# Performance work log

Measured on AMD Instinct MI355X. Metric: run time of the kernel, lower is better.

Reference implementation:

```python
import jax, jax.numpy as jnp
import numpy as np

N = 200000   # lane-graph nodes
C = 128      # n_map
S = 6        # num_scales
EP = 100000  # edges per pre/suc scale
EL = 25000   # left/right edges
EPS = 1e-5


def gn1(x, g, b):
    # GroupNorm(1, C) over shape [N, C]: normalize per node across channels, affine per channel
    mu = jnp.mean(x, axis=-1, keepdims=True)
    var = jnp.mean(jnp.square(x - mu), axis=-1, keepdims=True)
    return (x - mu) * jax.lax.rsqrt(var + EPS) * g + b


def setup_inputs() -> dict:
    key = jax.random.key(0)
    ks = jax.random.split(key, 32)
    f = lambda i, shape, s=1.0: jax.random.normal(ks[i], shape, dtype=jnp.float32) * s
    sc = 1.0 / np.sqrt(C)
    inp = {
        'control':   f(0, (N,)),
        'turn':      f(1, (N, 2)),
        'intersect': f(2, (N,)),
        'ctrs':      f(3, (N, 2)),
        'feats':     f(4, (N, 2)),
        'pre':   jax.random.randint(ks[5], (S, 2, EP), 0, N, dtype=jnp.int32),
        'suc':   jax.random.randint(ks[6], (S, 2, EP), 0, N, dtype=jnp.int32),
        'left':  jax.random.randint(ks[7], (2, EL), 0, N, dtype=jnp.int32),
        'right': jax.random.randint(ks[8], (2, EL), 0, N, dtype=jnp.int32),
        # input branch: Linear(2,C)+b, ReLU, Linear(C,C,no bias)+GroupNorm(1,C)
        'w_in1': f(9, (2, C), 0.7), 'b_in1': jnp.zeros((C,), jnp.float32),
        'w_in2': f(10, (C, C), sc), 'gn_in_g': jnp.ones((C,), jnp.float32), 'gn_in_b': jnp.zeros((C,), jnp.float32),
        # seg branch
        'w_seg1': f(11, (2, C), 0.7), 'b_seg1': jnp.zeros((C,), jnp.float32),
        'w_seg2': f(12, (C, C), sc), 'gn_seg_g': jnp.ones((C,), jnp.float32), 'gn_seg_b': jnp.zeros((C,), jnp.float32),
        # meta: Linear(C+4,C,no bias)+GN+ReLU
        'w_meta': f(13, (C + 4, C), sc), 'gn_meta_g': jnp.ones((C,), jnp.float32), 'gn_meta_b': jnp.zeros((C,), jnp.float32),
        # fuse dict, 4 layers
        'ctr_w':   f(14, (4, C, C), sc),
        'pre_w':   f(15, (4, S, C, C), sc),
        'suc_w':   f(16, (4, S, C, C), sc),
        'left_w':  f(17, (4, C, C), sc),
        'right_w': f(18, (4, C, C), sc),
        'norm_g': jnp.ones((4, C), jnp.float32), 'norm_b': jnp.zeros((4, C), jnp.float32),
        'ctr2_w': f(19, (4, C, C), sc),
        'ctr2_g': jnp.ones((4, C), jnp.float32), 'ctr2_b': jnp.zeros((4, C), jnp.float32),
    }
    return inp


def reference(control, turn, intersect, ctrs, feats, pre, suc, left, right,
              w_in1, b_in1, w_in2, gn_in_g, gn_in_b,
              w_seg1, b_seg1, w_seg2, gn_seg_g, gn_seg_b,
              w_meta, gn_meta_g, gn_meta_b,
              ctr_w, pre_w, suc_w, left_w, right_w,
              norm_g, norm_b, ctr2_w, ctr2_g, ctr2_b):
    # input / seg branches
    a = gn1(jax.nn.relu(ctrs @ w_in1 + b_in1) @ w_in2, gn_in_g, gn_in_b)
    b = gn1(jax.nn.relu(feats @ w_seg1 + b_seg1) @ w_seg2, gn_seg_g, gn_seg_b)
    feat = jax.nn.relu(a + b)
    # meta fuse
    meta = jnp.concatenate([feat, turn, control[:, None], intersect[:, None]], axis=1)
    feat = jax.nn.relu(gn1(meta @ w_meta, gn_meta_g, gn_meta_b))
    res = feat
    for i in range(4):
        temp = feat @ ctr_w[i]
        # multi-scale pre/suc: gather -> per-scale linear -> scatter-add
        pre_msg = jnp.einsum('sec,scd->sed', feat[pre[:, 1]], pre_w[i])   # [S,EP,C]
        temp = temp.at[pre[:, 0].reshape(-1)].add(pre_msg.reshape(-1, C))
        suc_msg = jnp.einsum('sec,scd->sed', feat[suc[:, 1]], suc_w[i])
        temp = temp.at[suc[:, 0].reshape(-1)].add(suc_msg.reshape(-1, C))
        temp = temp.at[left[0]].add(feat[left[1]] @ left_w[i])
        temp = temp.at[right[0]].add(feat[right[1]] @ right_w[i])
        feat = jax.nn.relu(gn1(temp, norm_g[i], norm_b[i]))
        feat = gn1(feat @ ctr2_w[i], ctr2_g[i], ctr2_b[i])
        feat = jax.nn.relu(feat + res)
        res = feat
    return (feat, ctrs)
```

## Files before the change

### kernel.cpp

```cpp
#include <hip/hip_runtime.h>

#define N_NODES 200000
#define CDIM 128
#define NSCALE 6
#define NEP 100000
#define NEL 25000
#define NCLS 14
#define NCHUNK 196
#define MROWS 64

typedef unsigned short u16;
typedef unsigned int u32;

using fragAB = __attribute__((ext_vector_type(8))) short;
using fragC  = __attribute__((ext_vector_type(4))) float;

enum { P_PLAIN = 0, P_TWO = 1, P_META = 2 };
enum { E_GN = 1, E_RELU = 2 };

__device__ __forceinline__ float4 ld4(const float* p) { return *(const float4*)p; }

__device__ __forceinline__ u16 f2bf(float f) {
  u32 u = __builtin_bit_cast(u32, f);
  u = (u + 0x7fff + ((u >> 16) & 1)) >> 16;
  return (u16)u;
}
__device__ __forceinline__ u32 pk2(float a, float b) {
  return (u32)f2bf(a) | ((u32)f2bf(b) << 16);
}
__device__ __forceinline__ float bflo(u32 u) { return __builtin_bit_cast(float, u << 16); }
__device__ __forceinline__ float bfhi(u32 u) { return __builtin_bit_cast(float, u & 0xffff0000u); }

__device__ __forceinline__ void acc16(float* s, uint4 a, uint4 b) {
  s[0] += bflo(a.x); s[1] += bfhi(a.x); s[2]  += bflo(a.y); s[3]  += bfhi(a.y);
  s[4] += bflo(a.z); s[5] += bfhi(a.z); s[6]  += bflo(a.w); s[7]  += bfhi(a.w);
  s[8] += bflo(b.x); s[9] += bfhi(b.x); s[10] += bflo(b.y); s[11] += bfhi(b.y);
  s[12] += bflo(b.z); s[13] += bfhi(b.z); s[14] += bflo(b.w); s[15] += bfhi(b.w);
}

__host__ __device__ constexpr int idx_base(int c) {
  return (c < 12) ? c * NEP : 12 * NEP + (c - 12) * NEL;
}

__device__ __forceinline__ int wslot(int li, int c) {
  if (c < 0)  return 2 + li;
  if (c < 6)  return 18 + li * 6 + c;
  if (c < 12) return 42 + li * 6 + (c - 6);
  return (c == 12) ? (10 + li) : (14 + li);
}

template<int PRO, int EPI>
__global__ __launch_bounds__(256)
void mm_k(int M, int Kp,
          const float* __restrict__ Af, const float* __restrict__ A2f,
          const float* __restrict__ e0, const float* __restrict__ e1, const float* __restrict__ e2,
          const u16* __restrict__ Wt,
          float* __restrict__ Y, u16* __restrict__ Yb,
          const float* __restrict__ gn_g, const float* __restrict__ gn_b)
{
  constexpr int LSTR = 56;
  __shared__ u16 As[128 * LSTR];
  __shared__ u16 Bs[128 * LSTR];

  const int tid = threadIdx.x;
  const int lane = tid & 63, wid = tid >> 6;
  const int wm = (wid >> 1) * 64, wn = (wid & 1) * 64;
  const int q = lane >> 4, l16 = lane & 15;
  const int row0 = blockIdx.x * 128;
  const int srow = tid >> 1, shalf = tid & 1;

  fragC acc[4][4];
  #pragma unroll
  for (int i = 0; i < 4; i++)
    #pragma unroll
    for (int j = 0; j < 4; j++)
      #pragma unroll
      for (int e = 0; e < 4; e++) acc[i][j][e] = 0.0f;

  const int sgrow = row0 + srow;
  const bool svalid = (sgrow < M);
  float x0 = 0.f, x1 = 0.f, mx = 0.f, my = 0.f, mc = 0.f, mi = 0.f;
  if constexpr (PRO == P_TWO) {
    if (svalid) { x0 = Af[(size_t)sgrow * 2]; x1 = Af[(size_t)sgrow * 2 + 1]; }
  }
  if constexpr (PRO == P_META) {
    if (svalid) { mx = e0[(size_t)sgrow * 2]; my = e0[(size_t)sgrow * 2 + 1]; mc = e1[sgrow]; mi = e2[sgrow]; }
  }

  const int nk = Kp >> 5;
  for (int kt = 0; kt < nk; ++kt) {
    const int k0 = kt * 32 + shalf * 16;
    {
      u16* adst = &As[srow * LSTR + shalf * 16];
      float v[16];
      #pragma unroll
      for (int j = 0; j < 16; j++) v[j] = 0.f;
      if constexpr (PRO == P_TWO) {
        #pragma unroll
        for (int j0 = 0; j0 < 16; j0 += 4) {
          float4 wa = ld4(e0 + k0 + j0);
          float4 wb = ld4(e0 + 128 + k0 + j0);
          float4 bb = ld4(e1 + k0 + j0);
          v[j0]     = fmaxf(0.f, fmaf(x0, wa.x, fmaf(x1, wb.x, bb.x)));
          v[j0 + 1] = fmaxf(0.f, fmaf(x0, wa.y, fmaf(x1, wb.y, bb.y)));
          v[j0 + 2] = fmaxf(0.f, fmaf(x0, wa.z, fmaf(x1, wb.z, bb.z)));
          v[j0 + 3] = fmaxf(0.f, fmaf(x0, wa.w, fmaf(x1, wb.w, bb.w)));
        }
      } else {
        if (svalid) {
          if (k0 < 128) {
            const float* sa = Af + (size_t)sgrow * 128 + k0;
            const float* sb = A2f + (size_t)sgrow * 128 + k0;
            #pragma unroll
            for (int j0 = 0; j0 < 16; j0 += 4) {
              float4 a = ld4(sa + j0), b = ld4(sb + j0);
              v[j0]     = fmaxf(0.f, a.x + b.x);
              v[j0 + 1] = fmaxf(0.f, a.y + b.y);
              v[j0 + 2] = fmaxf(0.f, a.z + b.z);
              v[j0 + 3] = fmaxf(0.f, a.w + b.w);
            }
          } else {
            #pragma unroll
            for (int j = 0; j < 16; j++) {
              const int kk = k0 + j - 128;
              v[j] = (kk == 0) ? mx : (kk == 1) ? my : (kk == 2) ? mc : (kk == 3) ? mi : 0.f;
            }
          }
        }
      }
      u32 p[8];
      #pragma unroll
      for (int j = 0; j < 8; j++) p[j] = pk2(v[2 * j], v[2 * j + 1]);
      *(uint4*)adst = make_uint4(p[0], p[1], p[2], p[3]);
      *(uint4*)(adst + 8) = make_uint4(p[4], p[5], p[6], p[7]);
    }
    {
      const u16* s = Wt + (size_t)srow * Kp + k0;
      uint4 b0 = *(const uint4*)s, b1 = *(const uint4*)(s + 8);
      u16* bdst = &Bs[srow * LSTR + shalf * 16];
      *(uint4*)bdst = b0; *(uint4*)(bdst + 8) = b1;
    }
    __syncthreads();
    fragAB af[4], bf[4];
    #pragma unroll
    for (int t = 0; t < 4; t++) af[t] = *(const fragAB*)&As[(wm + t * 16 + l16) * LSTR + q * 8];
    #pragma unroll
    for (int t = 0; t < 4; t++) bf[t] = *(const fragAB*)&Bs[(wn + t * 16 + l16) * LSTR + q * 8];
    #pragma unroll
    for (int mt = 0; mt < 4; mt++)
      #pragma unroll
      for (int nt = 0; nt < 4; nt++)
        acc[mt][nt] = __builtin_amdgcn_mfma_f32_16x16x32_bf16(af[mt], bf[nt], acc[mt][nt], 0, 0, 0);
    __syncthreads();
  }

  __shared__ float2 red[128][2];
  __shared__ float2 stats[128];
  #pragma unroll
  for (int mt = 0; mt < 4; mt++)
    #pragma unroll
    for (int r = 0; r < 4; r++) {
      float s1 = acc[mt][0][r] + acc[mt][1][r] + acc[mt][2][r] + acc[mt][3][r];
      float s2 = acc[mt][0][r] * acc[mt][0][r] + acc[mt][1][r] * acc[mt][1][r]
               + acc[mt][2][r] * acc[mt][2][r] + acc[mt][3][r] * acc[mt][3][r];
      #pragma unroll
      for (int off = 1; off < 16; off <<= 1) {
        s1 += __shfl_xor(s1, off, 64);
        s2 += __shfl_xor(s2, off, 64);
      }
      if (l16 == 0) red[wm + mt * 16 + q * 4 + r][wid & 1] = make_float2(s1, s2);
    }
  __syncthreads();
  if (tid < 128) {
    const float2 p0 = red[tid][0], p1 = red[tid][1];
    const float m = (p0.x + p1.x) * (1.0f / 128.0f);
    const float var = (p0.y + p1.y) * (1.0f / 128.0f) - m * m;
    stats[tid] = make_float2(m, rsqrtf(var + 1e-5f));
  }
  __syncthreads();
  float gl[4], bl[4];
  #pragma unroll
  for (int nt = 0; nt < 4; nt++) {
    gl[nt] = gn_g[wn + nt * 16 + l16];
    bl[nt] = gn_b[wn + nt * 16 + l16];
  }
  #pragma unroll
  for (int mt = 0; mt < 4; mt++)
    #pragma unroll
    for (int r = 0; r < 4; r++) {
      const int rl = wm + mt * 16 + q * 4 + r;
      const int grow = row0 + rl;
      if (grow >= M) continue;
      const float2 st = stats[rl];
      #pragma unroll
      for (int nt = 0; nt < 4; nt++) {
        const int col = wn + nt * 16 + l16;
        float v = (acc[mt][nt][r] - st.x) * st.y * gl[nt] + bl[nt];
        if constexpr ((EPI & E_RELU) != 0) v = fmaxf(v, 0.f);
        if (Y)  Y[(size_t)grow * 128 + col] = v;
        if (Yb) Yb[(size_t)grow * 128 + col] = f2bf(v);
      }
    }
}

__global__ __launch_bounds__(256, 4)
void layer_k(const u16* __restrict__ Fin, u16* __restrict__ Fout,
             float* __restrict__ outf,
             const int* __restrict__ ptrs, const int* __restrict__ idxs,
             const u16* __restrict__ Wt, int li,
             const float* __restrict__ g1, const float* __restrict__ b1,
             const float* __restrict__ g2, const float* __restrict__ b2)
{
  __shared__ u16 ldsA[MROWS * 128];
  __shared__ u16 Bsb[128 * 32];
  __shared__ u16 ends[NCLS][MROWS];
  __shared__ int cbase[NCLS];
  __shared__ int ccnt[NCLS];
  __shared__ int idxC[2][256];

  float2* red   = (float2*)Bsb;
  float2* stats = (float2*)(Bsb + 512);

  const int tid = threadIdx.x;
  const int lane = tid & 63, wid = tid >> 6;
  const int wm = (wid >> 1) * 32, wn = (wid & 1) * 64;
  const int q = lane >> 4, l16 = lane & 15;
  const int row0 = blockIdx.x * MROWS;
  const int row8 = tid >> 3;
  const int goff = (tid & 7) * 16;

  auto swzA = [&](int row, int colu) -> u16* {
    u32 b = (u32)(row * 256 + colu * 2) ^ ((u32)(row & 7) << 4);
    return (u16*)((char*)ldsA + b);
  };
  auto swzB = [&](int row, int colu) -> u16* {
    u32 b = (u32)(row * 64 + colu * 2) ^ ((((u32)((row >> 1) ^ (row >> 3))) & 3u) << 4);
    return (u16*)((char*)Bsb + b);
  };

  fragC acc[2][4];
  #pragma unroll
  for (int i = 0; i < 2; i++)
    #pragma unroll
    for (int j = 0; j < 4; j++)
      #pragma unroll
      for (int e = 0; e < 4; e++) acc[i][j][e] = 0.0f;

  if (tid < NCLS) {
    const int* pc = ptrs + (size_t)tid * (N_NODES + 1);
    const int b = row0 ? pc[row0 - 1] : 0;
    const int hiRow = (row0 + MROWS - 1 < N_NODES) ? (row0 + MROWS - 1) : (N_NODES - 1);
    cbase[tid] = b;
    ccnt[tid] = pc[hiRow] - b;
  }
  __syncthreads();

  #pragma unroll 1
  for (int t = tid; t < NCLS * MROWS; t += 256) {
    const int c = t / MROWS, r = t % MROWS;
    const int grow = row0 + r;
    const int* pc = ptrs + (size_t)c * (N_NODES + 1);
    const int gr = (grow < N_NODES) ? grow : (N_NODES - 1);
    ends[c][r] = (u16)(pc[gr] - cbase[c]);
  }
  {
    const int srow4 = tid >> 2, q4 = tid & 3;
    const int sgrow = row0 + srow4;
    uint4 a[4];
    #pragma unroll
    for (int j = 0; j < 4; j++) a[j] = make_uint4(0, 0, 0, 0);
    if (sgrow < N_NODES) {
      const u16* s = Fin + (size_t)sgrow * 128 + q4 * 32;
      #pragma unroll
      for (int j = 0; j < 4; j++) a[j] = ((const uint4*)s)[j];
    }
    #pragma unroll
    for (int j = 0; j < 4; j++) *(uint4*)swzA(srow4, q4 * 32 + j * 8) = a[j];
  }
  {
    const int m = (ccnt[0] < 256) ? ccnt[0] : 256;
    if (tid < m) idxC[0][tid] = idxs[idx_base(0) + cbase[0] + tid];
  }

  const int srowB = tid >> 1, shalf = tid & 1;

  {
    const u16* W = Wt + (size_t)(2 + li) * 16384;
    uint4 pb0, pb1;
    {
      const u16* ws = W + (size_t)srowB * 128 + shalf * 16;
      pb0 = *(const uint4*)ws; pb1 = *(const uint4*)(ws + 8);
    }
    __syncthreads();
    #pragma unroll
    for (int kt = 0; kt < 4; ++kt) {
      *(uint4*)swzB(srowB, shalf * 16) = pb0;
      *(uint4*)swzB(srowB, shalf * 16 + 8) = pb1;
      if (kt < 3) {
        const u16* ws = W + (size_t)srowB * 128 + (kt + 1) * 32 + shalf * 16;
        pb0 = *(const uint4*)ws; pb1 = *(const uint4*)(ws + 8);
      }
      __syncthreads();
      fragAB af[2], bf[4];
      #pragma unroll
      for (int t = 0; t < 2; t++) af[t] = *(const fragAB*)swzA(wm + t * 16 + l16, kt * 32 + q * 8);
      #pragma unroll
      for (int t = 0; t < 4; t++) bf[t] = *(const fragAB*)swzB(wn + t * 16 + l16, q * 8);
      #pragma unroll
      for (int mt = 0; mt < 2; mt++)
        #pragma unroll
        for (int nt = 0; nt < 4; nt++)
          acc[mt][nt] = __builtin_amdgcn_mfma_f32_16x16x32_bf16(af[mt], bf[nt], acc[mt][nt], 0, 0, 0);
      __syncthreads();
    }
  }

  #pragma unroll 1
  for (int c = 0; c < NCLS; ++c) {
    const u16* W = Wt + (size_t)wslot(li, c) * 16384;
    const int cur = c & 1;
    if (c + 1 < NCLS) {
      const int m = (ccnt[c + 1] < 256) ? ccnt[c + 1] : 256;
      if (tid < m) idxC[cur ^ 1][tid] = idxs[idx_base(c + 1) + cbase[c + 1] + tid];
    }
    const int* icg = idxs + idx_base(c) + cbase[c];

    #pragma unroll 1
    for (int grp = 0; grp < 2; ++grp) {
      const int lrow = grp * 32 + row8;
      const int lo = lrow ? (int)ends[c][lrow - 1] : 0;
      const int hi = (int)ends[c][lrow];
      float s[16];
      #pragma unroll
      for (int j = 0; j < 16; j++) s[j] = 0.f;
      int p = lo;
      #pragma unroll 1
      for (; p + 2 <= hi; p += 2) {
        const int s0 = (p     < 256) ? idxC[cur][p]     : icg[p];
        const int s1 = (p + 1 < 256) ? idxC[cur][p + 1] : icg[p + 1];
        const u16* sp0 = Fin + (size_t)s0 * 128 + goff;
        const u16* sp1 = Fin + (size_t)s1 * 128 + goff;
        uint4 a0 = ((const uint4*)sp0)[0], a1 = ((const uint4*)sp0)[1];
        uint4 b0 = ((const uint4*)sp1)[0], b1 = ((const uint4*)sp1)[1];
        acc16(s, a0, a1);
        acc16(s, b0, b1);
      }
      if (p < hi) {
        const int s0 = (p < 256) ? idxC[cur][p] : icg[p];
        const u16* sp = Fin + (size_t)s0 * 128 + goff;
        acc16(s, ((const uint4*)sp)[0], ((const uint4*)sp)[1]);
      }
      u32 pk[8];
      #pragma unroll
      for (int j = 0; j < 8; j++) pk[j] = pk2(s[2 * j], s[2 * j + 1]);
      *(uint4*)swzA(lrow, goff)     = make_uint4(pk[0], pk[1], pk[2], pk[3]);
      *(uint4*)swzA(lrow, goff + 8) = make_uint4(pk[4], pk[5], pk[6], pk[7]);
    }

    uint4 pb0, pb1;
    {
      const u16* ws = W + (size_t)srowB * 128 + shalf * 16;
      pb0 = *(const uint4*)ws; pb1 = *(const uint4*)(ws + 8);
    }
    __syncthreads();

    #pragma unroll
    for (int kt = 0; kt < 4; ++kt) {
      *(uint4*)swzB(srowB, shalf * 16) = pb0;
      *(uint4*)swzB(srowB, shalf * 16 + 8) = pb1;
      if (kt < 3) {
        const u16* ws = W + (size_t)srowB * 128 + (kt + 1) * 32 + shalf * 16;
        pb0 = *(const uint4*)ws; pb1 = *(const uint4*)(ws + 8);
      }
      __syncthreads();
      fragAB af[2], bf[4];
      #pragma unroll
      for (int t = 0; t < 2; t++) af[t] = *(const fragAB*)swzA(wm + t * 16 + l16, kt * 32 + q * 8);
      #pragma unroll
      for (int t = 0; t < 4; t++) bf[t] = *(const fragAB*)swzB(wn + t * 16 + l16, q * 8);
      #pragma unroll
      for (int mt = 0; mt < 2; mt++)
        #pragma unroll
        for (int nt = 0; nt < 4; nt++)
          acc[mt][nt] = __builtin_amdgcn_mfma_f32_16x16x32_bf16(af[mt], bf[nt], acc[mt][nt], 0, 0, 0);
      __syncthreads();
    }
  }

  #pragma unroll
  for (int mt = 0; mt < 2; mt++)
    #pragma unroll
    for (int r = 0; r < 4; r++) {
      float s1 = acc[mt][0][r] + acc[mt][1][r] + acc[mt][2][r] + acc[mt][3][r];
      float s2 = acc[mt][0][r] * acc[mt][0][r] + acc[mt][1][r] * acc[mt][1][r]
               + acc[mt][2][r] * acc[mt][2][r] + acc[mt][3][r] * acc[mt][3][r];
      #pragma unroll
      for (int off = 1; off < 16; off <<= 1) {
        s1 += __shfl_xor(s1, off, 64);
        s2 += __shfl_xor(s2, off, 64);
      }
      if (l16 == 0) red[(wm + mt * 16 + q * 4 + r) * 2 + (wid & 1)] = make_float2(s1, s2);
    }
  __syncthreads();
  if (tid < MROWS) {
    const float2 p0 = red[tid * 2], p1 = red[tid * 2 + 1];
    const float m = (p0.x + p1.x) * (1.0f / 128.0f);
    const float var = (p0.y + p1.y) * (1.0f / 128.0f) - m * m;
    stats[tid] = make_float2(m, rsqrtf(var + 1e-5f));
  }
  __syncthreads();
  {
    float gl[4], bl[4];
    #pragma unroll
    for (int nt = 0; nt < 4; nt++) {
      gl[nt] = g1[wn + nt * 16 + l16];
      bl[nt] = b1[wn + nt * 16 + l16];
    }
    #pragma unroll
    for (int mt = 0; mt < 2; mt++)
      #pragma unroll
      for (int r = 0; r < 4; r++) {
        const int rl = wm + mt * 16 + q * 4 + r;
        const float2 st = stats[rl];
        #pragma unroll
        for (int nt = 0; nt < 4; nt++) {
          const int col = wn + nt * 16 + l16;
          const float v = fmaxf(0.f, (acc[mt][nt][r] - st.x) * st.y * gl[nt] + bl[nt]);
          *swzA(rl, col) = f2bf(v);
        }
      }
  }

  #pragma unroll
  for (int i = 0; i < 2; i++)
    #pragma unroll
    for (int j = 0; j < 4; j++)
      #pragma unroll
      for (int e = 0; e < 4; e++) acc[i][j][e] = 0.0f;
  {
    const u16* W2 = Wt + (size_t)(6 + li) * 16384;
    uint4 pb0, pb1;
    {
      const u16* ws = W2 + (size_t)srowB * 128 + shalf * 16;
      pb0 = *(const uint4*)ws; pb1 = *(const uint4*)(ws + 8);
    }
    __syncthreads();
    #pragma unroll
    for (int kt = 0; kt < 4; ++kt) {
      *(uint4*)swzB(srowB, shalf * 16) = pb0;
      *(uint4*)swzB(srowB, shalf * 16 + 8) = pb1;
      if (kt < 3) {
        const u16* ws = W2 + (size_t)srowB * 128 + (kt + 1) * 32 + shalf * 16;
        pb0 = *(const uint4*)ws; pb1 = *(const uint4*)(ws + 8);
      }
      __syncthreads();
      fragAB af[2], bf[4];
      #pragma unroll
      for (int t = 0; t < 2; t++) af[t] = *(const fragAB*)swzA(wm + t * 16 + l16, kt * 32 + q * 8);
      #pragma unroll
      for (int t = 0; t < 4; t++) bf[t] = *(const fragAB*)swzB(wn + t * 16 + l16, q * 8);
      #pragma unroll
      for (int mt = 0; mt < 2; mt++)
        #pragma unroll
        for (int nt = 0; nt < 4; nt++)
          acc[mt][nt] = __builtin_amdgcn_mfma_f32_16x16x32_bf16(af[mt], bf[nt], acc[mt][nt], 0, 0, 0);
      __syncthreads();
    }
  }

  #pragma unroll
  for (int mt = 0; mt < 2; mt++)
    #pragma unroll
    for (int r = 0; r < 4; r++) {
      float s1 = acc[mt][0][r] + acc[mt][1][r] + acc[mt][2][r] + acc[mt][3][r];
      float s2 = acc[mt][0][r] * acc[mt][0][r] + acc[mt][1][r] * acc[mt][1][r]
               + acc[mt][2][r] * acc[mt][2][r] + acc[mt][3][r] * acc[mt][3][r];
      #pragma unroll
      for (int off = 1; off < 16; off <<= 1) {
        s1 += __shfl_xor(s1, off, 64);
        s2 += __shfl_xor(s2, off, 64);
      }
      if (l16 == 0) red[(wm + mt * 16 + q * 4 + r) * 2 + (wid & 1)] = make_float2(s1, s2);
    }
  __syncthreads();
  if (tid < MROWS) {
    const float2 p0 = red[tid * 2], p1 = red[tid * 2 + 1];
    const float m = (p0.x + p1.x) * (1.0f / 128.0f);
    const float var = (p0.y + p1.y) * (1.0f / 128.0f) - m * m;
    stats[tid] = make_float2(m, rsqrtf(var + 1e-5f));
  }
  __syncthreads();
  {
    float gl[4], bl[4];
    #pragma unroll
    for (int nt = 0; nt < 4; nt++) {
      gl[nt] = g2[wn + nt * 16 + l16];
      bl[nt] = b2[wn + nt * 16 + l16];
    }
    #pragma unroll
    for (int mt = 0; mt < 2; mt++)
      #pragma unroll
      for (int r = 0; r < 4; r++) {
        const int rl = wm + mt * 16 + q * 4 + r;
        const int grow = row0 + rl;
        if (grow >= N_NODES) continue;
        const float2 st = stats[rl];
        #pragma unroll
        for (int nt = 0; nt < 4; nt++) {
          const int col = wn + nt * 16 + l16;
          const float res = bflo((u32)Fin[(size_t)grow * 128 + col]);
          float v = (acc[mt][nt][r] - st.x) * st.y * gl[nt] + bl[nt] + res;
          v = fmaxf(v, 0.f);
          if (outf) outf[(size_t)grow * 128 + col] = v;
          else      Fout[(size_t)grow * 128 + col] = f2bf(v);
        }
      }
  }
}

__global__ __launch_bounds__(256)
void prep_k(const float* __restrict__ in2, const float* __restrict__ seg2,
            const float* __restrict__ ctr, const float* __restrict__ ctr2,
            const float* __restrict__ lw, const float* __restrict__ rw,
            const float* __restrict__ pw, const float* __restrict__ sw,
            const float* __restrict__ meta, u16* __restrict__ Wt)
{
  const int id = blockIdx.x;
  const float* src;
  int K = 128, Kp = 128;
  if (id == 0) src = in2;
  else if (id == 1) src = seg2;
  else if (id < 6)  src = ctr  + (size_t)(id - 2) * 16384;
  else if (id < 10) src = ctr2 + (size_t)(id - 6) * 16384;
  else if (id < 14) src = lw   + (size_t)(id - 10) * 16384;
  else if (id < 18) src = rw   + (size_t)(id - 14) * 16384;
  else if (id < 42) src = pw   + (size_t)(id - 18) * 16384;
  else if (id < 66) src = sw   + (size_t)(id - 42) * 16384;
  else { src = meta; K = 132; Kp = 160; }
  u16* dst = Wt + (size_t)id * 16384;
  const int tot = 128 * Kp;
  for (int e = threadIdx.x; e < tot; e += 256) {
    const int n = e & 127, k = e >> 7;
    const float v = (k < K) ? src[(size_t)k * 128 + n] : 0.f;
    dst[(size_t)n * Kp + k] = f2bf(v);
  }
}

struct EdgeCfg { const int* dst[NCLS]; const int* src[NCLS]; int cnt[NCLS]; };

__global__ __launch_bounds__(256)
void hist_k(EdgeCfg cfg, int* __restrict__ ptrs)
{
  const int c = blockIdx.y;
  const int i = blockIdx.x * 256 + threadIdx.x;
  if (i < cfg.cnt[c]) atomicAdd(ptrs + (size_t)c * (N_NODES + 1) + cfg.dst[c][i], 1);
}

__global__ __launch_bounds__(256)
void scan1_k(const int* __restrict__ ptrs, int* __restrict__ part)
{
  const int c = blockIdx.y, b = blockIdx.x;
  const int* d = ptrs + (size_t)c * (N_NODES + 1) + b * 1024;
  const int rem = min(1024, N_NODES - b * 1024);
  int s = 0;
  for (int j = threadIdx.x; j < rem; j += 256) s += d[j];
  #pragma unroll
  for (int off = 32; off; off >>= 1) s += __shfl_xor(s, off, 64);
  __shared__ int r[4];
  if ((threadIdx.x & 63) == 0) r[threadIdx.x >> 6] = s;
  __syncthreads();
  if (threadIdx.x == 0) part[c * NCHUNK + b] = r[0] + r[1] + r[2] + r[3];
}

__global__ __launch_bounds__(64)
void scan2_k(int* __restrict__ part, int* __restrict__ ptrs)
{
  const int c = blockIdx.x;
  if (threadIdx.x) return;
  int* p = part + c * NCHUNK;
  int run = 0;
  for (int b = 0; b < NCHUNK; b++) { const int t = p[b]; p[b] = run; run += t; }
  ptrs[(size_t)c * (N_NODES + 1) + N_NODES] = run;
}

__global__ __launch_bounds__(256)
void scan3_k(int* __restrict__ ptrs, const int* __restrict__ part)
{
  const int c = blockIdx.y, b = blockIdx.x;
  int* d = ptrs + (size_t)c * (N_NODES + 1) + b * 1024;
  const int base = part[c * NCHUNK + b];
  const int gbase = b * 1024;
  const int i0 = threadIdx.x * 4;
  int v[4];
  #pragma unroll
  for (int j = 0; j < 4; j++) v[j] = (gbase + i0 + j < N_NODES) ? d[i0 + j] : 0;
  const int tsum = v[0] + v[1] + v[2] + v[3];
  __shared__ int sc[256];
  sc[threadIdx.x] = tsum;
  __syncthreads();
  #pragma unroll
  for (int off = 1; off < 256; off <<= 1) {
    const int t = (threadIdx.x >= off) ? sc[threadIdx.x - off] : 0;
    __syncthreads();
    sc[threadIdx.x] += t;
    __syncthreads();
  }
  int run = sc[threadIdx.x] - tsum + base;
  #pragma unroll
  for (int j = 0; j < 4; j++) {
    if (gbase + i0 + j < N_NODES) d[i0 + j] = run;
    run += v[j];
  }
}

__global__ __launch_bounds__(256)
void fill_k(EdgeCfg cfg, int* __restrict__ ptrs, int* __restrict__ idxs)
{
  const int c = blockIdx.y;
  const int i = blockIdx.x * 256 + threadIdx.x;
  if (i >= cfg.cnt[c]) return;
  const int d = cfg.dst[c][i];
  const int slot = atomicAdd(ptrs + (size_t)c * (N_NODES + 1) + d, 1);
  idxs[idx_base(c) + slot] = cfg.src[c][i];
}

__global__ __launch_bounds__(256)
void copy_k(const float* __restrict__ src, float* __restrict__ dst, int n)
{
  const int i = blockIdx.x * 256 + threadIdx.x;
  if (i < n) dst[i] = src[i];
}

extern "C" void kernel_launch(void* const* d_in, const int* in_sizes, int n_in,
                              void* d_out, int out_size, void* d_ws, size_t ws_size,
                              hipStream_t stream) {
  const float* control   = (const float*)d_in[0];
  const float* turn      = (const float*)d_in[1];
  const float* intersect = (const float*)d_in[2];
  const float* ctrs      = (const float*)d_in[3];
  const float* feats     = (const float*)d_in[4];
  const int*   pre   = (const int*)d_in[5];
  const int*   suc   = (const int*)d_in[6];
  const int*   left  = (const int*)d_in[7];
  const int*   right = (const int*)d_in[8];
  const float* w_in1   = (const float*)d_in[9];
  const float* b_in1   = (const float*)d_in[10];
  const float* w_in2   = (const float*)d_in[11];
  const float* gn_in_g = (const float*)d_in[12];
  const float* gn_in_b = (const float*)d_in[13];
  const float* w_seg1   = (const float*)d_in[14];
  const float* b_seg1   = (const float*)d_in[15];
  const float* w_seg2   = (const float*)d_in[16];
  const float* gn_seg_g = (const float*)d_in[17];
  const float* gn_seg_b = (const float*)d_in[18];
  const float* w_meta    = (const float*)d_in[19];
  const float* gn_meta_g = (const float*)d_in[20];
  const float* gn_meta_b = (const float*)d_in[21];
  const float* ctr_w   = (const float*)d_in[22];
  const float* pre_w   = (const float*)d_in[23];
  const float* suc_w   = (const float*)d_in[24];
  const float* left_w  = (const float*)d_in[25];
  const float* right_w = (const float*)d_in[26];
  const float* norm_g  = (const float*)d_in[27];
  const float* norm_b  = (const float*)d_in[28];
  const float* ctr2_w  = (const float*)d_in[29];
  const float* ctr2_g  = (const float*)d_in[30];
  const float* ctr2_b  = (const float*)d_in[31];

  const size_t NF = (size_t)N_NODES * CDIM;
  char* w = (char*)d_ws;
  float* Ta = (float*)w;  w += NF * 4;
  float* Tb = (float*)w;  w += NF * 4;
  u16* Fb0  = (u16*)w;    w += NF * 2;
  u16* Fb1  = (u16*)w;    w += NF * 2;
  u16* Wt   = (u16*)w;    w += (size_t)(67 * 16384 + 128 * 160) * 2;
  int* ptrs = (int*)w;    w += (size_t)NCLS * (N_NODES + 1) * 4;
  int* idxs = (int*)w;    w += (size_t)(12 * NEP + 2 * NEL) * 4;
  int* part = (int*)w;
  float* out = (float*)d_out;

  EdgeCfg cfg;
  for (int s = 0; s < NSCALE; s++) {
    cfg.dst[s] = pre + (size_t)s * 2 * NEP;     cfg.src[s] = pre + ((size_t)s * 2 + 1) * NEP;     cfg.cnt[s] = NEP;
    cfg.dst[6 + s] = suc + (size_t)s * 2 * NEP; cfg.src[6 + s] = suc + ((size_t)s * 2 + 1) * NEP; cfg.cnt[6 + s] = NEP;
  }
  cfg.dst[12] = left;  cfg.src[12] = left + NEL;  cfg.cnt[12] = NEL;
  cfg.dst[13] = right; cfg.src[13] = right + NEL; cfg.cnt[13] = NEL;

  const dim3 blk(256);
  const dim3 gN((N_NODES + 127) / 128);
  const dim3 gL((N_NODES + MROWS - 1) / MROWS);
  const dim3 gHist((NEP + 255) / 256, NCLS);
  const dim3 gScan(NCHUNK, NCLS);

  prep_k<<<dim3(67), blk, 0, stream>>>(w_in2, w_seg2, ctr_w, ctr2_w, left_w, right_w,
                                       pre_w, suc_w, w_meta, Wt);
  (void)hipMemsetAsync(ptrs, 0, (size_t)NCLS * (N_NODES + 1) * sizeof(int), stream);
  hist_k<<<gHist, blk, 0, stream>>>(cfg, ptrs);
  scan1_k<<<gScan, blk, 0, stream>>>(ptrs, part);
  scan2_k<<<dim3(NCLS), dim3(64), 0, stream>>>(part, ptrs);
  scan3_k<<<gScan, blk, 0, stream>>>(ptrs, part);
  fill_k<<<gHist, blk, 0, stream>>>(cfg, ptrs, idxs);

  mm_k<P_TWO, E_GN><<<gN, blk, 0, stream>>>(N_NODES, 128, ctrs, nullptr,
      w_in1, b_in1, nullptr, Wt + 0 * 16384, Ta, nullptr, gn_in_g, gn_in_b);
  mm_k<P_TWO, E_GN><<<gN, blk, 0, stream>>>(N_NODES, 128, feats, nullptr,
      w_seg1, b_seg1, nullptr, Wt + 1 * 16384, Tb, nullptr, gn_seg_g, gn_seg_b);
  mm_k<P_META, E_GN | E_RELU><<<gN, blk, 0, stream>>>(N_NODES, 160, Ta, Tb,
      turn, control, intersect, Wt + 66 * 16384, nullptr, Fb0, gn_meta_g, gn_meta_b);

  for (int i = 0; i < 4; i++) {
    const u16* Fin = (i & 1) ? Fb1 : Fb0;
    u16* Fout      = (i & 1) ? Fb0 : Fb1;
    layer_k<<<gL, blk, 0, stream>>>(Fin, Fout, (i == 3) ? out : nullptr,
        ptrs, idxs, Wt, i,
        norm_g + i * 128, norm_b + i * 128, ctr2_g + i * 128, ctr2_b + i * 128);
  }

  copy_k<<<dim3((2 * N_NODES + 255) / 256), blk, 0, stream>>>(ctrs, out + NF, 2 * N_NODES);
}
```

Baseline: 1.712 ms.

## Double-buffer weight tiles in LDS and store branch intermediates as bf16

In layer_k, the weight-tile staging now uses two LDS buffers. The next k-slice is written after the MFMAs on the current slice, which removes one __syncthreads per k-step. The per-class weight prefetch is also hoisted ahead of the neighbor gather so its global latency overlaps that work. Separately, the input and seg branch outputs Ta/Tb are written as bf16 instead of fp32 and read back as bf16 in the meta prologue, halving that traffic at some precision cost. The extra LDS buffer may reduce occupancy.

```diff
diff --git a/kernel.cpp b/kernel.cpp
--- a/kernel.cpp
+++ b/kernel.cpp
@@ -109,16 +109,17 @@
       } else {
         if (svalid) {
           if (k0 < 128) {
-            const float* sa = Af + (size_t)sgrow * 128 + k0;
-            const float* sb = A2f + (size_t)sgrow * 128 + k0;
+            const u16* sa = (const u16*)Af + (size_t)sgrow * 128 + k0;
+            const u16* sb = (const u16*)A2f + (size_t)sgrow * 128 + k0;
+            uint4 a0 = ((const uint4*)sa)[0], a1 = ((const uint4*)sa)[1];
+            uint4 b0 = ((const uint4*)sb)[0], b1 = ((const uint4*)sb)[1];
+            float s[16];
             #pragma unroll
-            for (int j0 = 0; j0 < 16; j0 += 4) {
-              float4 a = ld4(sa + j0), b = ld4(sb + j0);
-              v[j0]     = fmaxf(0.f, a.x + b.x);
-              v[j0 + 1] = fmaxf(0.f, a.y + b.y);
-              v[j0 + 2] = fmaxf(0.f, a.z + b.z);
-              v[j0 + 3] = fmaxf(0.f, a.w + b.w);
-            }
+            for (int j = 0; j < 16; j++) s[j] = 0.f;
+            acc16(s, a0, a1);
+            acc16(s, b0, b1);
+            #pragma unroll
+            for (int j = 0; j < 16; j++) v[j] = fmaxf(0.f, s[j]);
           } else {
             #pragma unroll
             for (int j = 0; j < 16; j++) {
@@ -212,14 +213,14 @@
              const float* __restrict__ g2, const float* __restrict__ b2)
 {
   __shared__ u16 ldsA[MROWS * 128];
-  __shared__ u16 Bsb[128 * 32];
+  __shared__ u16 Bsb[2][128 * 32];
   __shared__ u16 ends[NCLS][MROWS];
   __shared__ int cbase[NCLS];
   __shared__ int ccnt[NCLS];
   __shared__ int idxC[2][256];
 
-  float2* red   = (float2*)Bsb;
-  float2* stats = (float2*)(Bsb + 512);
+  float2* red   = (float2*)&Bsb[0][0];
+  float2* stats = (float2*)&Bsb[0][512];
 
   const int tid = threadIdx.x;
   const int lane = tid & 63, wid = tid >> 6;
@@ -233,9 +234,9 @@
     u32 b = (u32)(row * 256 + colu * 2) ^ ((u32)(row & 7) << 4);
     return (u16*)((char*)ldsA + b);
   };
-  auto swzB = [&](int row, int colu) -> u16* {
+  auto swzB = [&](int buf, int row, int colu) -> u16* {
     u32 b = (u32)(row * 64 + colu * 2) ^ ((((u32)((row >> 1) ^ (row >> 3))) & 3u) << 4);
-    return (u16*)((char*)Bsb + b);
+    return (u16*)((char*)&Bsb[buf][0] + b);
   };
 
   fragC acc[2][4];
@@ -286,31 +287,34 @@
 
   {
     const u16* W = Wt + (size_t)(2 + li) * 16384;
-    uint4 pb0, pb1;
     {
       const u16* ws = W + (size_t)srowB * 128 + shalf * 16;
-      pb0 = *(const uint4*)ws; pb1 = *(const uint4*)(ws + 8);
+      uint4 p0 = *(const uint4*)ws, p1 = *(const uint4*)(ws + 8);
+      *(uint4*)swzB(0, srowB, shalf * 16) = p0;
+      *(uint4*)swzB(0, srowB, shalf * 16 + 8) = p1;
     }
     __syncthreads();
     #pragma unroll
     for (int kt = 0; kt < 4; ++kt) {
-      *(uint4*)swzB(srowB, shalf * 16) = pb0;
-      *(uint4*)swzB(srowB, shalf * 16 + 8) = pb1;
+      uint4 pb0, pb1;
       if (kt < 3) {
         const u16* ws = W + (size_t)srowB * 128 + (kt + 1) * 32 + shalf * 16;
         pb0 = *(const uint4*)ws; pb1 = *(const uint4*)(ws + 8);
       }
-      __syncthreads();
       fragAB af[2], bf[4];
       #pragma unroll
       for (int t = 0; t < 2; t++) af[t] = *(const fragAB*)swzA(wm + t * 16 + l16, kt * 32 + q * 8);
       #pragma unroll
-      for (int t = 0; t < 4; t++) bf[t] = *(const fragAB*)swzB(wn + t * 16 + l16, q * 8);
+      for (int t = 0; t < 4; t++) bf[t] = *(const fragAB*)swzB(kt & 1, wn + t * 16 + l16, q * 8);
       #pragma unroll
       for (int mt = 0; mt < 2; mt++)
         #pragma unroll
         for (int nt = 0; nt < 4; nt++)
           acc[mt][nt] = __builtin_amdgcn_mfma_f32_16x16x32_bf16(af[mt], bf[nt], acc[mt][nt], 0, 0, 0);
+      if (kt < 3) {
+        *(uint4*)swzB((kt + 1) & 1, srowB, shalf * 16) = pb0;
+        *(uint4*)swzB((kt + 1) & 1, srowB, shalf * 16 + 8) = pb1;
+      }
       __syncthreads();
     }
   }
@@ -324,6 +328,12 @@
       if (tid < m) idxC[cur ^ 1][tid] = idxs[idx_base(c + 1) + cbase[c + 1] + tid];
     }
     const int* icg = idxs + idx_base(c) + cbase[c];
+
+    uint4 pc0, pc1;
+    {
+      const u16* ws = W + (size_t)srowB * 128 + shalf * 16;
+      pc0 = *(const uint4*)ws; pc1 = *(const uint4*)(ws + 8);
+    }
 
     #pragma unroll 1
     for (int grp = 0; grp < 2; ++grp) {
@@ -357,32 +367,32 @@
       *(uint4*)swzA(lrow, goff + 8) = make_uint4(pk[4], pk[5], pk[6], pk[7]);
     }
 
-    uint4 pb0, pb1;
-    {
-      const u16* ws = W + (size_t)srowB * 128 + shalf * 16;
-      pb0 = *(const uint4*)ws; pb1 = *(const uint4*)(ws + 8);
-    }
+    *(uint4*)swzB(0, srowB, shalf * 16) = pc0;
+    *(uint4*)swzB(0, srowB, shalf * 16 + 8) = pc1;
+
     __syncthreads();
 
     #pragma unroll
     for (int kt = 0; kt < 4; ++kt) {
-      *(uint4*)swzB(srowB, shalf * 16) = pb0;
-      *(uint4*)swzB(srowB, shalf * 16 + 8) = pb1;
+      uint4 pb0, pb1;
       if (kt < 3) {
         const u16* ws = W + (size_t)srowB * 128 + (kt + 1) * 32 + shalf * 16;
         pb0 = *(const uint4*)ws; pb1 = *(const uint4*)(ws + 8);
       }
-      __syncthreads();
       fragAB af[2], bf[4];
       #pragma unroll
       for (int t = 0; t < 2; t++) af[t] = *(const fragAB*)swzA(wm + t * 16 + l16, kt * 32 + q * 8);
       #pragma unroll
-      for (int t = 0; t < 4; t++) bf[t] = *(const fragAB*)swzB(wn + t * 16 + l16, q * 8);
+      for (int t = 0; t < 4; t++) bf[t] = *(const fragAB*)swzB(kt & 1, wn + t * 16 + l16, q * 8);
       #pragma unroll
       for (int mt = 0; mt < 2; mt++)
         #pragma unroll
         for (int nt = 0; nt < 4; nt++)
           acc[mt][nt] = __builtin_amdgcn_mfma_f32_16x16x32_bf16(af[mt], bf[nt], acc[mt][nt], 0, 0, 0);
+      if (kt < 3) {
+        *(uint4*)swzB((kt + 1) & 1, srowB, shalf * 16) = pb0;
+        *(uint4*)swzB((kt + 1) & 1, srowB, shalf * 16 + 8) = pb1;
+      }
       __syncthreads();
     }
   }
@@ -430,6 +440,7 @@
         }
       }
   }
+  __syncthreads();
 
   #pragma unroll
   for (int i = 0; i < 2; i++)
@@ -439,31 +450,34 @@
       for (int e = 0; e < 4; e++) acc[i][j][e] = 0.0f;
   {
     const u16* W2 = Wt + (size_t)(6 + li) * 16384;
-    uint4 pb0, pb1;
     {
       const u16* ws = W2 + (size_t)srowB * 128 + shalf * 16;
-      pb0 = *(const uint4*)ws; pb1 = *(const uint4*)(ws + 8);
+      uint4 p0 = *(const uint4*)ws, p1 = *(const uint4*)(ws + 8);
+      *(uint4*)swzB(0, srowB, shalf * 16) = p0;
+      *(uint4*)swzB(0, srowB, shalf * 16 + 8) = p1;
     }
     __syncthreads();
     #pragma unroll
     for (int kt = 0; kt < 4; ++kt) {
-      *(uint4*)swzB(srowB, shalf * 16) = pb0;
-      *(uint4*)swzB(srowB, shalf * 16 + 8) = pb1;
+      uint4 pb0, pb1;
       if (kt < 3) {
         const u16* ws = W2 + (size_t)srowB * 128 + (kt + 1) * 32 + shalf * 16;
         pb0 = *(const uint4*)ws; pb1 = *(const uint4*)(ws + 8);
       }
-      __syncthreads();
       fragAB af[2], bf[4];
       #pragma unroll
       for (int t = 0; t < 2; t++) af[t] = *(const fragAB*)swzA(wm + t * 16 + l16, kt * 32 + q * 8);
       #pragma unroll
-      for (int t = 0; t < 4; t++) bf[t] = *(const fragAB*)swzB(wn + t * 16 + l16, q * 8);
+      for (int t = 0; t < 4; t++) bf[t] = *(const fragAB*)swzB(kt & 1, wn + t * 16 + l16, q * 8);
       #pragma unroll
       for (int mt = 0; mt < 2; mt++)
         #pragma unroll
         for (int nt = 0; nt < 4; nt++)
           acc[mt][nt] = __builtin_amdgcn_mfma_f32_16x16x32_bf16(af[mt], bf[nt], acc[mt][nt], 0, 0, 0);
+      if (kt < 3) {
+        *(uint4*)swzB((kt + 1) & 1, srowB, shalf * 16) = pb0;
+        *(uint4*)swzB((kt + 1) & 1, srowB, shalf * 16 + 8) = pb1;
+      }
       __syncthreads();
     }
   }
@@ -669,8 +683,8 @@
 
   const size_t NF = (size_t)N_NODES * CDIM;
   char* w = (char*)d_ws;
-  float* Ta = (float*)w;  w += NF * 4;
-  float* Tb = (float*)w;  w += NF * 4;
+  u16* Ta   = (u16*)w;    w += NF * 2;
+  u16* Tb   = (u16*)w;    w += NF * 2;
   u16* Fb0  = (u16*)w;    w += NF * 2;
   u16* Fb1  = (u16*)w;    w += NF * 2;
   u16* Wt   = (u16*)w;    w += (size_t)(67 * 16384 + 128 * 160) * 2;
@@ -703,10 +717,11 @@
   fill_k<<<gHist, blk, 0, stream>>>(cfg, ptrs, idxs);
 
   mm_k<P_TWO, E_GN><<<gN, blk, 0, stream>>>(N_NODES, 128, ctrs, nullptr,
-      w_in1, b_in1, nullptr, Wt + 0 * 16384, Ta, nullptr, gn_in_g, gn_in_b);
+      w_in1, b_in1, nullptr, Wt + 0 * 16384, nullptr, Ta, gn_in_g, gn_in_b);
   mm_k<P_TWO, E_GN><<<gN, blk, 0, stream>>>(N_NODES, 128, feats, nullptr,
-      w_seg1, b_seg1, nullptr, Wt + 1 * 16384, Tb, nullptr, gn_seg_g, gn_seg_b);
-  mm_k<P_META, E_GN | E_RELU><<<gN, blk, 0, stream>>>(N_NODES, 160, Ta, Tb,
+      w_seg1, b_seg1, nullptr, Wt + 1 * 16384, nullptr, Tb, gn_seg_g, gn_seg_b);
+  mm_k<P_META, E_GN | E_RELU><<<gN, blk, 0, stream>>>(N_NODES, 160,
+      (const float*)Ta, (const float*)Tb,
       turn, control, intersect, Wt + 66 * 16384, nullptr, Fb0, gn_meta_g, gn_meta_b);
 
   for (int i = 0; i < 4; i++) {
```

After: 1.802 ms. +5.2%, slower.

## Fuse input, seg and meta GEMM branches into a single prologue kernel

Applied to the files above, without the earlier changes.

Replaces three separate mm_k launches with one kernel that computes both the input and seg branches per 128-row tile. It keeps their ReLU-summed result in swizzled shared memory as bf16, then runs the meta GEMM from LDS with the four meta scalars packed into an extra K tile. This removes two fp32 N×128 intermediate buffers and their global write and read traffic. In exchange the a+b sum is rounded to bf16 before use, and the larger LDS footprint may lower occupancy.

```diff
diff --git a/kernel.cpp b/kernel.cpp
--- a/kernel.cpp
+++ b/kernel.cpp
@@ -15,9 +15,6 @@
 using fragAB = __attribute__((ext_vector_type(8))) short;
 using fragC  = __attribute__((ext_vector_type(4))) float;
 
-enum { P_PLAIN = 0, P_TWO = 1, P_META = 2 };
-enum { E_GN = 1, E_RELU = 2 };
-
 __device__ __forceinline__ float4 ld4(const float* p) { return *(const float4*)p; }
 
 __device__ __forceinline__ u16 f2bf(float f) {
@@ -49,18 +46,25 @@
   return (c == 12) ? (10 + li) : (14 + li);
 }
 
-template<int PRO, int EPI>
 __global__ __launch_bounds__(256)
-void mm_k(int M, int Kp,
-          const float* __restrict__ Af, const float* __restrict__ A2f,
-          const float* __restrict__ e0, const float* __restrict__ e1, const float* __restrict__ e2,
-          const u16* __restrict__ Wt,
-          float* __restrict__ Y, u16* __restrict__ Yb,
-          const float* __restrict__ gn_g, const float* __restrict__ gn_b)
+void pro_k(const float* __restrict__ ctrs, const float* __restrict__ feats,
+           const float* __restrict__ turn, const float* __restrict__ control,
+           const float* __restrict__ intersect,
+           const float* __restrict__ w_in1, const float* __restrict__ b_in1,
+           const float* __restrict__ w_seg1, const float* __restrict__ b_seg1,
+           const u16* __restrict__ Wt,
+           u16* __restrict__ Fb0,
+           const float* __restrict__ gin_g, const float* __restrict__ gin_b,
+           const float* __restrict__ gseg_g, const float* __restrict__ gseg_b,
+           const float* __restrict__ gmeta_g, const float* __restrict__ gmeta_b)
 {
   constexpr int LSTR = 56;
+  __shared__ u16 Fa[128 * 128];
   __shared__ u16 As[128 * LSTR];
   __shared__ u16 Bs[128 * LSTR];
+  __shared__ u16 meta4[128][8];
+  __shared__ float2 red[128][2];
+  __shared__ float2 stats[128];
 
   const int tid = threadIdx.x;
   const int lane = tid & 63, wid = tid >> 6;
@@ -68,94 +72,176 @@
   const int q = lane >> 4, l16 = lane & 15;
   const int row0 = blockIdx.x * 128;
   const int srow = tid >> 1, shalf = tid & 1;
+  const int sgrow = row0 + srow;
+  const bool svalid = (sgrow < N_NODES);
+
+  auto swzA = [&](int row, int colu) -> u16* {
+    u32 b = (u32)(row * 256 + colu * 2) ^ ((u32)(row & 7) << 4);
+    return (u16*)((char*)Fa + b);
+  };
+
+  if (tid < 128) {
+    const int g = row0 + tid;
+    float m0 = 0.f, m1 = 0.f, m2 = 0.f, m3 = 0.f;
+    if (g < N_NODES) {
+      m0 = turn[2 * (size_t)g]; m1 = turn[2 * (size_t)g + 1];
+      m2 = control[g]; m3 = intersect[g];
+    }
+    *(uint4*)&meta4[tid][0] = make_uint4(pk2(m0, m1), pk2(m2, m3), 0, 0);
+  }
 
   fragC acc[4][4];
-  #pragma unroll
-  for (int i = 0; i < 4; i++)
-    #pragma unroll
-    for (int j = 0; j < 4; j++)
-      #pragma unroll
-      for (int e = 0; e < 4; e++) acc[i][j][e] = 0.0f;
-
-  const int sgrow = row0 + srow;
-  const bool svalid = (sgrow < M);
-  float x0 = 0.f, x1 = 0.f, mx = 0.f, my = 0.f, mc = 0.f, mi = 0.f;
-  if constexpr (PRO == P_TWO) {
-    if (svalid) { x0 = Af[(size_t)sgrow * 2]; x1 = Af[(size_t)sgrow * 2 + 1]; }
-  }
-  if constexpr (PRO == P_META) {
-    if (svalid) { mx = e0[(size_t)sgrow * 2]; my = e0[(size_t)sgrow * 2 + 1]; mc = e1[sgrow]; mi = e2[sgrow]; }
-  }
-
-  const int nk = Kp >> 5;
-  for (int kt = 0; kt < nk; ++kt) {
-    const int k0 = kt * 32 + shalf * 16;
+
+  #pragma unroll 1
+  for (int st = 0; st < 2; ++st) {
+    const float* Xf = st ? feats : ctrs;
+    const float* w1 = st ? w_seg1 : w_in1;
+    const float* bb = st ? b_seg1 : b_in1;
+    const u16* W2   = Wt + (size_t)st * 16384;
+    const float* gg = st ? gseg_g : gin_g;
+    const float* gb = st ? gseg_b : gin_b;
+
+    float x0 = 0.f, x1 = 0.f;
+    if (svalid) { x0 = Xf[2 * (size_t)sgrow]; x1 = Xf[2 * (size_t)sgrow + 1]; }
+
+    #pragma unroll
+    for (int i = 0; i < 4; i++)
+      #pragma unroll
+      for (int j = 0; j < 4; j++)
+        #pragma unroll
+        for (int e = 0; e < 4; e++) acc[i][j][e] = 0.0f;
+
+    #pragma unroll 1
+    for (int kt = 0; kt < 4; ++kt) {
+      const int k0 = kt * 32 + shalf * 16;
+      {
+        float v[16];
+        #pragma unroll
+        for (int j0 = 0; j0 < 16; j0 += 4) {
+          float4 wa = ld4(w1 + k0 + j0);
+          float4 wb = ld4(w1 + 128 + k0 + j0);
+          float4 bv = ld4(bb + k0 + j0);
+          v[j0]     = fmaxf(0.f, fmaf(x0, wa.x, fmaf(x1, wb.x, bv.x)));
+          v[j0 + 1] = fmaxf(0.f, fmaf(x0, wa.y, fmaf(x1, wb.y, bv.y)));
+          v[j0 + 2] = fmaxf(0.f, fmaf(x0, wa.z, fmaf(x1, wb.z, bv.z)));
+          v[j0 + 3] = fmaxf(0.f, fmaf(x0, wa.w, fmaf(x1, wb.w, bv.w)));
+        }
+        u32 p[8];
+        #pragma unroll
+        for (int j = 0; j < 8; j++) p[j] = pk2(v[2 * j], v[2 * j + 1]);
+        u16* adst = &As[srow * LSTR + shalf * 16];
+        *(uint4*)adst = make_uint4(p[0], p[1], p[2], p[3]);
+        *(uint4*)(adst + 8) = make_uint4(p[4], p[5], p[6], p[7]);
+      }
+      {
+        const u16* s = W2 + (size_t)srow * 128 + k0;
+        uint4 b0 = *(const uint4*)s, b1 = *(const uint4*)(s + 8);
+        u16* bdst = &Bs[srow * LSTR + shalf * 16];
+        *(uint4*)bdst = b0; *(uint4*)(bdst + 8) = b1;
+      }
+      __syncthreads();
+      fragAB af[4], bf[4];
+      #pragma unroll
+      for (int t = 0; t < 4; t++) af[t] = *(const fragAB*)&As[(wm + t * 16 + l16) * LSTR + q * 8];
+      #pragma unroll
+      for (int t = 0; t < 4; t++) bf[t] = *(const fragAB*)&Bs[(wn + t * 16 + l16) * LSTR + q * 8];
+      #pragma unroll
+      for (int mt = 0; mt < 4; mt++)
+        #pragma unroll
+        for (int nt = 0; nt < 4; nt++)
+          acc[mt][nt] = __builtin_amdgcn_mfma_f32_16x16x32_bf16(af[mt], bf[nt], acc[mt][nt], 0, 0, 0);
+      __syncthreads();
+    }
+
+    #pragma unroll
+    for (int mt = 0; mt < 4; mt++)
+      #pragma unroll
+      for (int r = 0; r < 4; r++) {
+        float s1 = acc[mt][0][r] + acc[mt][1][r] + acc[mt][2][r] + acc[mt][3][r];
+        float s2 = acc[mt][0][r] * acc[mt][0][r] + acc[mt][1][r] * acc[mt][1][r]
+                 + acc[mt][2][r] * acc[mt][2][r] + acc[mt][3][r] * acc[mt][3][r];
+        #pragma unroll
+        for (int off = 1; off < 16; off <<= 1) {
+          s1 += __shfl_xor(s1, off, 64);
+          s2 += __shfl_xor(s2, off, 64);
+        }
+        if (l16 == 0) red[wm + mt * 16 + q * 4 + r][wid & 1] = make_float2(s1, s2);
+      }
+    __syncthreads();
+    if (tid < 128) {
+      const float2 p0 = red[tid][0], p1 = red[tid][1];
+      const float m = (p0.x + p1.x) * (1.0f / 128.0f);
+      const float var = (p0.y + p1.y) * (1.0f / 128.0f) - m * m;
+      stats[tid] = make_float2(m, rsqrtf(var + 1e-5f));
+    }
+    __syncthreads();
     {
-      u16* adst = &As[srow * LSTR + shalf * 16];
-      float v[16];
-      #pragma unroll
-      for (int j = 0; j < 16; j++) v[j] = 0.f;
-      if constexpr (PRO == P_TWO) {
-        #pragma unroll
-        for (int j0 = 0; j0 < 16; j0 += 4) {
-          float4 wa = ld4(e0 + k0 + j0);
-          float4 wb = ld4(e0 + 128 + k0 + j0);
-          float4 bb = ld4(e1 + k0 + j0);
-          v[j0]     = fmaxf(0.f, fmaf(x0, wa.x, fmaf(x1, wb.x, bb.x)));
-          v[j0 + 1] = fmaxf(0.f, fmaf(x0, wa.y, fmaf(x1, wb.y, bb.y)));
-          v[j0 + 2] = fmaxf(0.f, fmaf(x0, wa.z, fmaf(x1, wb.z, bb.z)));
-          v[j0 + 3] = fmaxf(0.f, fmaf(x0, wa.w, fmaf(x1, wb.w, bb.w)));
-        }
-      } else {
-        if (svalid) {
-          if (k0 < 128) {
-            const float* sa = Af + (size_t)sgrow * 128 + k0;
-            const float* sb = A2f + (size_t)sgrow * 128 + k0;
-            #pragma unroll
-            for (int j0 = 0; j0 < 16; j0 += 4) {
-              float4 a = ld4(sa + j0), b = ld4(sb + j0);
-              v[j0]     = fmaxf(0.f, a.x + b.x);
-              v[j0 + 1] = fmaxf(0.f, a.y + b.y);
-              v[j0 + 2] = fmaxf(0.f, a.z + b.z);
-              v[j0 + 3] = fmaxf(0.f, a.w + b.w);
-            }
-          } else {
-            #pragma unroll
-            for (int j = 0; j < 16; j++) {
-              const int kk = k0 + j - 128;
-              v[j] = (kk == 0) ? mx : (kk == 1) ? my : (kk == 2) ? mc : (kk == 3) ? mi : 0.f;
+      float gl[4], bl[4];
+      #pragma unroll
+      for (int nt = 0; nt < 4; nt++) {
+        gl[nt] = gg[wn + nt * 16 + l16];
+        bl[nt] = gb[wn + nt * 16 + l16];
+      }
+      #pragma unroll
+      for (int mt = 0; mt < 4; mt++)
+        #pragma unroll
+        for (int r = 0; r < 4; r++) {
+          const int rl = wm + mt * 16 + q * 4 + r;
+          const float2 stv = stats[rl];
+          #pragma unroll
+          for (int nt = 0; nt < 4; nt++) {
+            const int col = wn + nt * 16 + l16;
+            const float gnv = (acc[mt][nt][r] - stv.x) * stv.y * gl[nt] + bl[nt];
+            if (st == 0) {
+              *swzA(rl, col) = f2bf(gnv);
+            } else {
+              const float aval = bflo((u32)*swzA(rl, col));
+              *swzA(rl, col) = f2bf(fmaxf(0.f, aval + gnv));
             }
           }
         }
-      }
-      u32 p[8];
-      #pragma unroll
-      for (int j = 0; j < 8; j++) p[j] = pk2(v[2 * j], v[2 * j + 1]);
-      *(uint4*)adst = make_uint4(p[0], p[1], p[2], p[3]);
-      *(uint4*)(adst + 8) = make_uint4(p[4], p[5], p[6], p[7]);
-    }
-    {
-      const u16* s = Wt + (size_t)srow * Kp + k0;
-      uint4 b0 = *(const uint4*)s, b1 = *(const uint4*)(s + 8);
-      u16* bdst = &Bs[srow * LSTR + shalf * 16];
-      *(uint4*)bdst = b0; *(uint4*)(bdst + 8) = b1;
-    }
-    __syncthreads();
-    fragAB af[4], bf[4];
-    #pragma unroll
-    for (int t = 0; t < 4; t++) af[t] = *(const fragAB*)&As[(wm + t * 16 + l16) * LSTR + q * 8];
-    #pragma unroll
-    for (int t = 0; t < 4; t++) bf[t] = *(const fragAB*)&Bs[(wn + t * 16 + l16) * LSTR + q * 8];
-    #pragma unroll
-    for (int mt = 0; mt < 4; mt++)
-      #pragma unroll
-      for (int nt = 0; nt < 4; nt++)
-        acc[mt][nt] = __builtin_amdgcn_mfma_f32_16x16x32_bf16(af[mt], bf[nt], acc[mt][nt], 0, 0, 0);
-    __syncthreads();
-  }
-
-  __shared__ float2 red[128][2];
-  __shared__ float2 stats[128];
+    }
+  }
+
+  #pragma unroll
+  for (int i = 0; i < 4; i++)
+    #pragma unroll
+    for (int j = 0; j < 4; j++)
+      #pragma unroll
+      for (int e = 0; e < 4; e++) acc[i][j][e] = 0.0f;
+  {
+    const u16* W66 = Wt + (size_t)66 * 16384;
+    #pragma unroll 1
+    for (int kt = 0; kt < 5; ++kt) {
+      const int k0 = kt * 32 + shalf * 16;
+      {
+        const u16* s = W66 + (size_t)srow * 160 + k0;
+        uint4 b0 = *(const uint4*)s, b1 = *(const uint4*)(s + 8);
+        u16* bdst = &Bs[srow * LSTR + shalf * 16];
+        *(uint4*)bdst = b0; *(uint4*)(bdst + 8) = b1;
+      }
+      __syncthreads();
+      fragAB af[4], bf[4];
+      if (kt < 4) {
+        #pragma unroll
+        for (int t = 0; t < 4; t++) af[t] = *(const fragAB*)swzA(wm + t * 16 + l16, kt * 32 + q * 8);
+      } else {
+        #pragma unroll
+        for (int t = 0; t < 4; t++)
+          af[t] = (q == 0) ? *(const fragAB*)&meta4[wm + t * 16 + l16][0]
+                           : __builtin_bit_cast(fragAB, make_uint4(0, 0, 0, 0));
+      }
+      #pragma unroll
+      for (int t = 0; t < 4; t++) bf[t] = *(const fragAB*)&Bs[(wn + t * 16 + l16) * LSTR + q * 8];
+      #pragma unroll
+      for (int mt = 0; mt < 4; mt++)
+        #pragma unroll
+        for (int nt = 0; nt < 4; nt++)
+          acc[mt][nt] = __builtin_amdgcn_mfma_f32_16x16x32_bf16(af[mt], bf[nt], acc[mt][nt], 0, 0, 0);
+      __syncthreads();
+    }
+  }
+
   #pragma unroll
   for (int mt = 0; mt < 4; mt++)
     #pragma unroll
@@ -178,29 +264,29 @@
     stats[tid] = make_float2(m, rsqrtf(var + 1e-5f));
   }
   __syncthreads();
-  float gl[4], bl[4];
-  #pragma unroll
-  for (int nt = 0; nt < 4; nt++) {
-    gl[nt] = gn_g[wn + nt * 16 + l16];
-    bl[nt] = gn_b[wn + nt * 16 + l16];
-  }
-  #pragma unroll
-  for (int mt = 0; mt < 4; mt++)
-    #pragma unroll
-    for (int r = 0; r < 4; r++) {
-      const int rl = wm + mt * 16 + q * 4 + r;
-      const int grow = row0 + rl;
-      if (grow >= M) continue;
-      const float2 st = stats[rl];
-      #pragma unroll
-      for (int nt = 0; nt < 4; nt++) {
-        const int col = wn + nt * 16 + l16;
-        float v = (acc[mt][nt][r] - st.x) * st.y * gl[nt] + bl[nt];
-        if constexpr ((EPI & E_RELU) != 0) v = fmaxf(v, 0.f);
-        if (Y)  Y[(size_t)grow * 128 + col] = v;
-        if (Yb) Yb[(size_t)grow * 128 + col] = f2bf(v);
-      }
-    }
+  {
+    float gl[4], bl[4];
+    #pragma unroll
+    for (int nt = 0; nt < 4; nt++) {
+      gl[nt] = gmeta_g[wn + nt * 16 + l16];
+      bl[nt] = gmeta_b[wn + nt * 16 + l16];
+    }
+    #pragma unroll
+    for (int mt = 0; mt < 4; mt++)
+      #pragma unroll
+      for (int r = 0; r < 4; r++) {
+        const int rl = wm + mt * 16 + q * 4 + r;
+        const int grow = row0 + rl;
+        if (grow >= N_NODES) continue;
+        const float2 stv = stats[rl];
+        #pragma unroll
+        for (int nt = 0; nt < 4; nt++) {
+          const int col = wn + nt * 16 + l16;
+          const float v = fmaxf(0.f, (acc[mt][nt][r] - stv.x) * stv.y * gl[nt] + bl[nt]);
+          Fb0[(size_t)grow * 128 + col] = f2bf(v);
+        }
+      }
+  }
 }
 
 __global__ __launch_bounds__(256, 4)
@@ -669,8 +755,6 @@
 
   const size_t NF = (size_t)N_NODES * CDIM;
   char* w = (char*)d_ws;
-  float* Ta = (float*)w;  w += NF * 4;
-  float* Tb = (float*)w;  w += NF * 4;
   u16* Fb0  = (u16*)w;    w += NF * 2;
   u16* Fb1  = (u16*)w;    w += NF * 2;
   u16* Wt   = (u16*)w;    w += (size_t)(67 * 16384 + 128 * 160) * 2;
@@ -702,12 +786,9 @@
   scan3_k<<<gScan, blk, 0, stream>>>(ptrs, part);
   fill_k<<<gHist, blk, 0, stream>>>(cfg, ptrs, idxs);
 
-  mm_k<P_TWO, E_GN><<<gN, blk, 0, stream>>>(N_NODES, 128, ctrs, nullptr,
-      w_in1, b_in1, nullptr, Wt + 0 * 16384, Ta, nullptr, gn_in_g, gn_in_b);
-  mm_k<P_TWO, E_GN><<<gN, blk, 0, stream>>>(N_NODES, 128, feats, nullptr,
-      w_seg1, b_seg1, nullptr, Wt + 1 * 16384, Tb, nullptr, gn_seg_g, gn_seg_b);
-  mm_k<P_META, E_GN | E_RELU><<<gN, blk, 0, stream>>>(N_NODES, 160, Ta, Tb,
-      turn, control, intersect, Wt + 66 * 16384, nullptr, Fb0, gn_meta_g, gn_meta_b);
+  pro_k<<<gN, blk, 0, stream>>>(ctrs, feats, turn, control, intersect,
+      w_in1, b_in1, w_seg1, b_seg1, Wt, Fb0,
+      gn_in_g, gn_in_b, gn_seg_g, gn_seg_b, gn_meta_g, gn_meta_b);
 
   for (int i = 0; i < 4; i++) {
     const u16* Fin = (i & 1) ? Fb1 : Fb0;
```

Result: no change. 1.746 ms (+2.0%).
